# Kernel tuning notes

Measured on AMD Instinct MI355X. Metric: run time of the kernel, lower is better.

The kernel has to match this reference:

```python
import jax, jax.numpy as jnp
import numpy as np

N = 50000
E = 800000
HIDDEN = 128
NUM_HEADS = 8
D_HEAD = HIDDEN // NUM_HEADS


def setup_inputs() -> dict:
    key = jax.random.key(0)
    ks = jax.random.split(key, 12)
    sc = 1.0 / np.sqrt(HIDDEN)
    inp = {
        "h": jax.random.normal(ks[0], (N, HIDDEN), dtype=jnp.float32),
        "rows": jax.random.randint(ks[1], (E,), 0, N, dtype=jnp.int32),
        "cols": jax.random.randint(ks[2], (E,), 0, N, dtype=jnp.int32),
        "Wq": jax.random.normal(ks[3], (HIDDEN, HIDDEN), dtype=jnp.float32) * sc,
        "bq": jax.random.normal(ks[4], (HIDDEN,), dtype=jnp.float32) * sc,
        "Wk": jax.random.normal(ks[5], (HIDDEN, HIDDEN), dtype=jnp.float32) * sc,
        "bk": jax.random.normal(ks[6], (HIDDEN,), dtype=jnp.float32) * sc,
        "Wv": jax.random.normal(ks[7], (HIDDEN, HIDDEN), dtype=jnp.float32) * sc,
        "bv": jax.random.normal(ks[8], (HIDDEN,), dtype=jnp.float32) * sc,
        "Wo": jax.random.normal(ks[9], (HIDDEN, HIDDEN), dtype=jnp.float32) * sc,
        "bo": jax.random.normal(ks[10], (HIDDEN,), dtype=jnp.float32) * sc,
    }
    return inp


def reference(h, rows, cols, Wq, bq, Wk, bk, Wv, bv, Wo, bo):
    n = h.shape[0]
    scaling = D_HEAD ** (-0.5)
    # projections; torch-style reshape splits hidden as (d_head, num_heads)
    q = ((h @ Wq.T + bq).reshape(n, D_HEAD, NUM_HEADS)) * scaling
    k = (h @ Wk.T + bk).reshape(n, D_HEAD, NUM_HEADS)
    v = (h @ Wv.T + bv).reshape(n, D_HEAD, NUM_HEADS)
    # SDDMM: per-edge, per-head score = q[row] . k[col]   -> [E, H]
    scores = jnp.einsum("edh,edh->eh", q[rows], k[cols])
    # row-wise (destination) stable softmax over variable-degree neighborhoods
    m = jax.ops.segment_max(scores, rows, num_segments=n)  # [N, H]
    e = jnp.exp(scores - m[rows])
    s = jax.ops.segment_sum(e, rows, num_segments=n)  # [N, H]
    attn = e / s[rows]  # [E, H]
    # SpMM: out[i] = sum_{(i,j) in E} attn[e] * v[j]
    out = jax.ops.segment_sum(attn[:, None, :] * v[cols], rows, num_segments=n)
    return out.reshape(n, HIDDEN) @ Wo.T + bo
```

## Files before the change

### kernel.cpp

```cpp
#include <hip/hip_runtime.h>
#include <math.h>

#define N_NODES 50000
#define N_EDGES 800000
#define HID 128
#define CAP 64
#define EPT 8
#define SCAT_THREADS (N_EDGES / EPT)
#define SCAT_BLOCKS ((SCAT_THREADS + 255) / 256)
#define QKV_BLOCKS  ((N_NODES + 31) / 32)
#define ATTN_BLOCKS ((N_NODES + 3) / 4)
#define OUT_BLOCKS  ((N_NODES + 63) / 64)

typedef _Float16 f16_t;
typedef f16_t f16x8 __attribute__((ext_vector_type(8)));
typedef f16_t f16x2 __attribute__((ext_vector_type(2)));
typedef float f32x4 __attribute__((ext_vector_type(4)));

__device__ __forceinline__ ushort f2h_bits(float x) {
    union { f16_t h; ushort u; } c; c.h = (f16_t)x; return c.u;
}
__device__ __forceinline__ f16x2 as_h2(uint u) {
    union { uint u_; f16x2 h; } c; c.u_ = u; return c.h;
}
__device__ __forceinline__ f16x8 cvt8(const float* p) {
    float4 f0 = *(const float4*)p;
    float4 f1 = *(const float4*)(p + 4);
    f16x8 r;
    r[0] = (f16_t)f0.x; r[1] = (f16_t)f0.y; r[2] = (f16_t)f0.z; r[3] = (f16_t)f0.w;
    r[4] = (f16_t)f1.x; r[5] = (f16_t)f1.y; r[6] = (f16_t)f1.z; r[7] = (f16_t)f1.w;
    return r;
}

__global__ __launch_bounds__(256) void scatter(
    const int* __restrict__ rows, const int* __restrict__ cols,
    int* __restrict__ cnt, ushort* __restrict__ slots)
{
    const int t = blockIdx.x * 256 + threadIdx.x;
    if (t >= SCAT_THREADS) return;
    const int4* r4 = (const int4*)rows + (size_t)t * 2;
    const int4* c4 = (const int4*)cols + (size_t)t * 2;
    int4 ra = r4[0], rb = r4[1];
    int4 ca = c4[0], cb = c4[1];
    const int r[8] = {ra.x, ra.y, ra.z, ra.w, rb.x, rb.y, rb.z, rb.w};
    const int c[8] = {ca.x, ca.y, ca.z, ca.w, cb.x, cb.y, cb.z, cb.w};
    int p[8];
#pragma unroll
    for (int u = 0; u < 8; ++u)
        p[u] = atomicAdd(&cnt[r[u] << 4], 1);
#pragma unroll
    for (int u = 0; u < 8; ++u)
        if (p[u] < CAP) slots[(size_t)r[u] * CAP + p[u]] = (ushort)c[u];
}

__global__ __launch_bounds__(256) void gemm_qkv(
    const float* __restrict__ h,
    const float* __restrict__ Wq, const float* __restrict__ Wk,
    const float* __restrict__ Wv,
    const float* __restrict__ bq, const float* __restrict__ bk,
    const float* __restrict__ bv,
    uint* __restrict__ qp, uint2* __restrict__ kv)
{
    const int lane = threadIdx.x & 63;
    const int wid  = threadIdx.x >> 6;
    const int mrow = lane & 15;
    const int quad = lane >> 4;
    const int rb   = blockIdx.x * 32;

    f16x8 a[2][4];
#pragma unroll
    for (int s = 0; s < 2; ++s) {
        if (rb + s * 16 >= N_NODES) break;
        const float* src = h + (size_t)(rb + s * 16 + mrow) * HID + quad * 8;
#pragma unroll
        for (int kc = 0; kc < 4; ++kc) a[s][kc] = cvt8(src + kc * 32);
    }

    const int c0 = wid * 32 + mrow;
    const int c1 = c0 + 16;

    f16x8 bfr[2][4];
    f32x4 accq[2][2], acck[2][2], accv[2][2];

#define LOAD_B(W)                                                       \
    _Pragma("unroll")                                                   \
    for (int kc = 0; kc < 4; ++kc) {                                    \
        bfr[0][kc] = cvt8((W) + c0 * HID + kc * 32 + quad * 8);         \
        bfr[1][kc] = cvt8((W) + c1 * HID + kc * 32 + quad * 8);         \
    }
#define RUN_MFMA(dst)                                                   \
    _Pragma("unroll")                                                   \
    for (int s = 0; s < 2; ++s) {                                       \
        dst[s][0] = (f32x4){0.f, 0.f, 0.f, 0.f};                        \
        dst[s][1] = (f32x4){0.f, 0.f, 0.f, 0.f};                        \
        if (rb + s * 16 >= N_NODES) continue;                           \
        _Pragma("unroll")                                               \
        for (int kc = 0; kc < 4; ++kc) {                                \
            dst[s][0] = __builtin_amdgcn_mfma_f32_16x16x32_f16(         \
                a[s][kc], bfr[0][kc], dst[s][0], 0, 0, 0);              \
            dst[s][1] = __builtin_amdgcn_mfma_f32_16x16x32_f16(         \
                a[s][kc], bfr[1][kc], dst[s][1], 0, 0, 0);              \
        }                                                               \
    }

    LOAD_B(Wq); RUN_MFMA(accq);
    LOAD_B(Wk); RUN_MFMA(acck);
    LOAD_B(Wv); RUN_MFMA(accv);
#undef LOAD_B
#undef RUN_MFMA

    const float bq0 = bq[c0], bq1 = bq[c1];
    const float bk0 = bk[c0], bk1 = bk[c1];
    const float bv0 = bv[c0], bv1 = bv[c1];
    const bool  lo  = (mrow & 8) == 0;
    const int   i   = mrow & 7;

#pragma unroll
    for (int s = 0; s < 2; ++s) {
        if (rb + s * 16 >= N_NODES) break;
#pragma unroll
        for (int r = 0; r < 4; ++r) {
            const size_t orow = rb + s * 16 + quad * 4 + r;
            uint q0 = f2h_bits((accq[s][0][r] + bq0) * 0.25f);
            uint q1 = f2h_bits((accq[s][1][r] + bq1) * 0.25f);
            uint k0 = f2h_bits(acck[s][0][r] + bk0);
            uint k1 = f2h_bits(acck[s][1][r] + bk1);
            uint v0 = f2h_bits(accv[s][0][r] + bv0);
            uint v1 = f2h_bits(accv[s][1][r] + bv1);
            uint q0p = __shfl_xor(q0, 8), q1p = __shfl_xor(q1, 8);
            uint k0p = __shfl_xor(k0, 8), k1p = __shfl_xor(k1, 8);
            uint v0p = __shfl_xor(v0, 8), v1p = __shfl_xor(v1, 8);
            if (lo) {
                const size_t base = orow * 64 + 16 * wid + i;
                qp[base]     = q0 | (q0p << 16);
                qp[base + 8] = q1 | (q1p << 16);
                kv[base]     = make_uint2(k0 | (k0p << 16), v0 | (v0p << 16));
                kv[base + 8] = make_uint2(k1 | (k1p << 16), v1 | (v1p << 16));
            }
        }
    }
}

__device__ __forceinline__ void edge_acc(uint2 rr, f16x2 qh,
                                         float& l, float& Oa, float& Ob)
{
    float p = __builtin_amdgcn_fdot2(as_h2(rr.x), qh, 0.f, false);
    p += __shfl_xor(p, 8);
    p += __shfl_xor(p, 16);
    p += __shfl_xor(p, 32);
    float ex = __expf(p);
    f16x2 vh = as_h2(rr.y);
    l  += ex;
    Oa += ex * (float)vh[0];
    Ob += ex * (float)vh[1];
}

__global__ __launch_bounds__(256) void attn(
    const uint* __restrict__ qp, const uint2* __restrict__ kv,
    const int* __restrict__ cnt, const ushort* __restrict__ slots,
    ushort* __restrict__ ao)
{
    const int lane = threadIdx.x & 63;
    const int node = blockIdx.x * 4 + (threadIdx.x >> 6);
    if (node >= N_NODES) return;

    const f16x2 qh = as_h2(qp[(size_t)node * 64 + lane]);

    int deg = cnt[node << 4];
    if (deg > CAP) deg = CAP;
    const int myslot = (lane < deg) ? (int)slots[(size_t)node * CAP + lane] : 0;

    float ls[4] = {0.f, 0.f, 0.f, 0.f};
    float Oa[4] = {0.f, 0.f, 0.f, 0.f};
    float Ob[4] = {0.f, 0.f, 0.f, 0.f};

    int j = 0;
    for (; j + 4 <= deg; j += 4) {
        int s0 = __shfl(myslot, j);
        int s1 = __shfl(myslot, j + 1);
        int s2 = __shfl(myslot, j + 2);
        int s3 = __shfl(myslot, j + 3);
        uint2 r0 = kv[(size_t)s0 * 64 + lane];
        uint2 r1 = kv[(size_t)s1 * 64 + lane];
        uint2 r2 = kv[(size_t)s2 * 64 + lane];
        uint2 r3 = kv[(size_t)s3 * 64 + lane];
        edge_acc(r0, qh, ls[0], Oa[0], Ob[0]);
        edge_acc(r1, qh, ls[1], Oa[1], Ob[1]);
        edge_acc(r2, qh, ls[2], Oa[2], Ob[2]);
        edge_acc(r3, qh, ls[3], Oa[3], Ob[3]);
    }
    for (; j < deg; ++j) {
        int s = __shfl(myslot, j);
        uint2 rr = kv[(size_t)s * 64 + lane];
        edge_acc(rr, qh, ls[0], Oa[0], Ob[0]);
    }

    const float l  = (ls[0] + ls[1]) + (ls[2] + ls[3]);
    const float O0 = (Oa[0] + Oa[1]) + (Oa[2] + Oa[3]);
    const float O1 = (Ob[0] + Ob[1]) + (Ob[2] + Ob[3]);
    const float inv = (l > 0.f) ? 1.f / l : 0.f;

    const int ce = 32 * (lane >> 4) + 16 * ((lane >> 3) & 1) + (lane & 7);
    ao[(size_t)node * HID + ce]     = f2h_bits(O0 * inv);
    ao[(size_t)node * HID + ce + 8] = f2h_bits(O1 * inv);
}

__global__ __launch_bounds__(256) void gemm_out(
    const ushort* __restrict__ A, const float* __restrict__ Wo,
    const float* __restrict__ bias, float* __restrict__ out)
{
    const int lane = threadIdx.x & 63;
    const int wid  = threadIdx.x >> 6;
    const int mrow = lane & 15;
    const int quad = lane >> 4;
    const int rb   = blockIdx.x * 64;

    const int c0 = wid * 32 + mrow;
    const int c1 = c0 + 16;

    f16x8 bfr[2][4];
#pragma unroll
    for (int kc = 0; kc < 4; ++kc) {
        bfr[0][kc] = cvt8(Wo + c0 * HID + kc * 32 + quad * 8);
        bfr[1][kc] = cvt8(Wo + c1 * HID + kc * 32 + quad * 8);
    }

    f32x4 acc[4][2];
#pragma unroll
    for (int s = 0; s < 4; ++s) {
        acc[s][0] = (f32x4){0.f, 0.f, 0.f, 0.f};
        acc[s][1] = (f32x4){0.f, 0.f, 0.f, 0.f};
    }

#pragma unroll
    for (int s = 0; s < 4; ++s) {
        if (rb + s * 16 >= N_NODES) break;
        const ushort* ap = A + (size_t)(rb + s * 16 + mrow) * HID + quad * 8;
        f16x8 a0 = *(const f16x8*)(ap);
        f16x8 a1 = *(const f16x8*)(ap + 32);
        f16x8 a2 = *(const f16x8*)(ap + 64);
        f16x8 a3 = *(const f16x8*)(ap + 96);
        acc[s][0] = __builtin_amdgcn_mfma_f32_16x16x32_f16(a0, bfr[0][0], acc[s][0], 0, 0, 0);
        acc[s][1] = __builtin_amdgcn_mfma_f32_16x16x32_f16(a0, bfr[1][0], acc[s][1], 0, 0, 0);
        acc[s][0] = __builtin_amdgcn_mfma_f32_16x16x32_f16(a1, bfr[0][1], acc[s][0], 0, 0, 0);
        acc[s][1] = __builtin_amdgcn_mfma_f32_16x16x32_f16(a1, bfr[1][1], acc[s][1], 0, 0, 0);
        acc[s][0] = __builtin_amdgcn_mfma_f32_16x16x32_f16(a2, bfr[0][2], acc[s][0], 0, 0, 0);
        acc[s][1] = __builtin_amdgcn_mfma_f32_16x16x32_f16(a2, bfr[1][2], acc[s][1], 0, 0, 0);
        acc[s][0] = __builtin_amdgcn_mfma_f32_16x16x32_f16(a3, bfr[0][3], acc[s][0], 0, 0, 0);
        acc[s][1] = __builtin_amdgcn_mfma_f32_16x16x32_f16(a3, bfr[1][3], acc[s][1], 0, 0, 0);
    }

#pragma unroll
    for (int t = 0; t < 2; ++t) {
        const int c = (t == 0) ? c0 : c1;
        const float bc = bias[c];
#pragma unroll
        for (int s = 0; s < 4; ++s) {
            if (rb + s * 16 >= N_NODES) break;
#pragma unroll
            for (int r = 0; r < 4; ++r) {
                const size_t orow = rb + s * 16 + quad * 4 + r;
                out[orow * HID + c] = acc[s][t][r] + bc;
            }
        }
    }
}

extern "C" void kernel_launch(void* const* d_in, const int* in_sizes, int n_in,
                              void* d_out, int out_size, void* d_ws, size_t ws_size,
                              hipStream_t stream)
{
    const float* h    = (const float*)d_in[0];
    const int*   rows = (const int*)  d_in[1];
    const int*   cols = (const int*)  d_in[2];
    const float* Wq   = (const float*)d_in[3];
    const float* bq   = (const float*)d_in[4];
    const float* Wk   = (const float*)d_in[5];
    const float* bk   = (const float*)d_in[6];
    const float* Wv   = (const float*)d_in[7];
    const float* bv   = (const float*)d_in[8];
    const float* Wo   = (const float*)d_in[9];
    const float* bo   = (const float*)d_in[10];
    float* out = (float*)d_out;

    char* ws = (char*)d_ws;
    uint*   qp    = (uint*)ws;    ws += (size_t)N_NODES * 64 * 4;
    uint2*  kv    = (uint2*)ws;   ws += (size_t)N_NODES * 64 * 8;
    ushort* ao    = (ushort*)ws;  ws += (size_t)N_NODES * HID * 2;
    int*    cnt   = (int*)ws;     ws += (size_t)N_NODES * 64;
    ushort* slots = (ushort*)ws;

    hipMemsetAsync(cnt, 0, (size_t)N_NODES * 64, stream);

    dim3 blk(256);
    scatter<<<SCAT_BLOCKS, blk, 0, stream>>>(rows, cols, cnt, slots);
    gemm_qkv<<<QKV_BLOCKS, blk, 0, stream>>>(h, Wq, Wk, Wv, bq, bk, bv, qp, kv);
    attn<<<ATTN_BLOCKS, blk, 0, stream>>>(qp, kv, cnt, slots, ao);
    gemm_out<<<OUT_BLOCKS, blk, 0, stream>>>(ao, Wo, bo, out);
}
```

Measured before the change: 256.1 us.

## Fuse fp16 pre-conversion of h and weights into scatter prep kernel, split QKV GEMM

Adds a combined prep kernel that runs the edge scatter alongside fp16 conversion of h and all four weight matrices, so the GEMMs load fp16 directly instead of converting fp32 on the fly. The QKV GEMM gets a second grid dimension so each wave computes one 16-column tile across Q, K and V, which doubles the block count and changes the per-wave output layout. The attention output column mapping is adjusted to match. The cost is an extra fp16 copy of h written to and read back from the workspace, and the QKV kernel now reloads the A tile once per y-block.

```diff
diff --git a/kernel.cpp b/kernel.cpp
--- a/kernel.cpp
+++ b/kernel.cpp
@@ -5,12 +5,16 @@
 #define N_EDGES 800000
 #define HID 128
 #define CAP 64
-#define EPT 8
-#define SCAT_THREADS (N_EDGES / EPT)
-#define SCAT_BLOCKS ((SCAT_THREADS + 255) / 256)
-#define QKV_BLOCKS  ((N_NODES + 31) / 32)
-#define ATTN_BLOCKS ((N_NODES + 3) / 4)
-#define OUT_BLOCKS  ((N_NODES + 63) / 64)
+
+#define SCAT_TH   (N_EDGES / 8)
+#define SCAT_BLK  ((SCAT_TH + 255) / 256)
+#define WCVT_BLK  64
+#define HCVT_BLK  (N_NODES * HID / 4 / 256)
+#define PREP_BLK  (SCAT_BLK + WCVT_BLK + HCVT_BLK)
+
+#define QKV_BX    ((N_NODES + 31) / 32)
+#define ATTN_BLK  ((N_NODES + 3) / 4)
+#define OUT_BLK   ((N_NODES + 63) / 64)
 
 typedef _Float16 f16_t;
 typedef f16_t f16x8 __attribute__((ext_vector_type(8)));
@@ -23,40 +27,56 @@
 __device__ __forceinline__ f16x2 as_h2(uint u) {
     union { uint u_; f16x2 h; } c; c.u_ = u; return c.h;
 }
-__device__ __forceinline__ f16x8 cvt8(const float* p) {
-    float4 f0 = *(const float4*)p;
-    float4 f1 = *(const float4*)(p + 4);
-    f16x8 r;
-    r[0] = (f16_t)f0.x; r[1] = (f16_t)f0.y; r[2] = (f16_t)f0.z; r[3] = (f16_t)f0.w;
-    r[4] = (f16_t)f1.x; r[5] = (f16_t)f1.y; r[6] = (f16_t)f1.z; r[7] = (f16_t)f1.w;
-    return r;
-}
-
-__global__ __launch_bounds__(256) void scatter(
+
+__global__ __launch_bounds__(256) void prep(
+    const float* __restrict__ h,
+    const float* __restrict__ Wq, const float* __restrict__ Wk,
+    const float* __restrict__ Wv, const float* __restrict__ Wo,
+    ushort* __restrict__ hf, ushort* __restrict__ wf,
     const int* __restrict__ rows, const int* __restrict__ cols,
     int* __restrict__ cnt, ushort* __restrict__ slots)
 {
-    const int t = blockIdx.x * 256 + threadIdx.x;
-    if (t >= SCAT_THREADS) return;
-    const int4* r4 = (const int4*)rows + (size_t)t * 2;
-    const int4* c4 = (const int4*)cols + (size_t)t * 2;
-    int4 ra = r4[0], rb = r4[1];
-    int4 ca = c4[0], cb = c4[1];
-    const int r[8] = {ra.x, ra.y, ra.z, ra.w, rb.x, rb.y, rb.z, rb.w};
-    const int c[8] = {ca.x, ca.y, ca.z, ca.w, cb.x, cb.y, cb.z, cb.w};
-    int p[8];
-#pragma unroll
-    for (int u = 0; u < 8; ++u)
-        p[u] = atomicAdd(&cnt[r[u] << 4], 1);
-#pragma unroll
-    for (int u = 0; u < 8; ++u)
-        if (p[u] < CAP) slots[(size_t)r[u] * CAP + p[u]] = (ushort)c[u];
+    const int b = blockIdx.x;
+    const int tid = threadIdx.x;
+
+    if (b < SCAT_BLK) {
+        const int t = b * 256 + tid;
+        if (t < SCAT_TH) {
+            const int4* r4 = (const int4*)rows + (size_t)t * 2;
+            const int4* c4 = (const int4*)cols + (size_t)t * 2;
+            int4 ra = r4[0], rb2 = r4[1];
+            int4 ca = c4[0], cb = c4[1];
+            const int r[8] = {ra.x, ra.y, ra.z, ra.w, rb2.x, rb2.y, rb2.z, rb2.w};
+            const int c[8] = {ca.x, ca.y, ca.z, ca.w, cb.x, cb.y, cb.z, cb.w};
+            int p[8];
+#pragma unroll
+            for (int u = 0; u < 8; ++u)
+                p[u] = atomicAdd(&cnt[r[u] << 4], 1);
+#pragma unroll
+            for (int u = 0; u < 8; ++u)
+                if (p[u] < CAP) slots[(size_t)r[u] * CAP + p[u]] = (ushort)c[u];
+        }
+    } else if (b < SCAT_BLK + WCVT_BLK) {
+        const int t = (b - SCAT_BLK) * 256 + tid;
+        const int m = t >> 12, i = t & 4095;
+        const float* src = (m == 0) ? Wq : (m == 1) ? Wk : (m == 2) ? Wv : Wo;
+        float4 f = ((const float4*)src)[i];
+        ushort4 o;
+        o.x = f2h_bits(f.x); o.y = f2h_bits(f.y);
+        o.z = f2h_bits(f.z); o.w = f2h_bits(f.w);
+        ((ushort4*)(wf + m * 16384))[i] = o;
+    } else {
+        const int t = (b - SCAT_BLK - WCVT_BLK) * 256 + tid;
+        float4 f = ((const float4*)h)[t];
+        ushort4 o;
+        o.x = f2h_bits(f.x); o.y = f2h_bits(f.y);
+        o.z = f2h_bits(f.z); o.w = f2h_bits(f.w);
+        ((ushort4*)hf)[t] = o;
+    }
 }
 
 __global__ __launch_bounds__(256) void gemm_qkv(
-    const float* __restrict__ h,
-    const float* __restrict__ Wq, const float* __restrict__ Wk,
-    const float* __restrict__ Wv,
+    const ushort* __restrict__ hf, const ushort* __restrict__ wf,
     const float* __restrict__ bq, const float* __restrict__ bk,
     const float* __restrict__ bv,
     uint* __restrict__ qp, uint2* __restrict__ kv)
@@ -66,79 +86,63 @@
     const int mrow = lane & 15;
     const int quad = lane >> 4;
     const int rb   = blockIdx.x * 32;
+    const int T    = blockIdx.y * 4 + wid;
+    const int c    = T * 16 + mrow;
 
     f16x8 a[2][4];
 #pragma unroll
     for (int s = 0; s < 2; ++s) {
-        if (rb + s * 16 >= N_NODES) break;
-        const float* src = h + (size_t)(rb + s * 16 + mrow) * HID + quad * 8;
-#pragma unroll
-        for (int kc = 0; kc < 4; ++kc) a[s][kc] = cvt8(src + kc * 32);
-    }
-
-    const int c0 = wid * 32 + mrow;
-    const int c1 = c0 + 16;
-
-    f16x8 bfr[2][4];
-    f32x4 accq[2][2], acck[2][2], accv[2][2];
-
-#define LOAD_B(W)                                                       \
-    _Pragma("unroll")                                                   \
-    for (int kc = 0; kc < 4; ++kc) {                                    \
-        bfr[0][kc] = cvt8((W) + c0 * HID + kc * 32 + quad * 8);         \
-        bfr[1][kc] = cvt8((W) + c1 * HID + kc * 32 + quad * 8);         \
-    }
-#define RUN_MFMA(dst)                                                   \
-    _Pragma("unroll")                                                   \
-    for (int s = 0; s < 2; ++s) {                                       \
-        dst[s][0] = (f32x4){0.f, 0.f, 0.f, 0.f};                        \
-        dst[s][1] = (f32x4){0.f, 0.f, 0.f, 0.f};                        \
-        if (rb + s * 16 >= N_NODES) continue;                           \
-        _Pragma("unroll")                                               \
-        for (int kc = 0; kc < 4; ++kc) {                                \
-            dst[s][0] = __builtin_amdgcn_mfma_f32_16x16x32_f16(         \
-                a[s][kc], bfr[0][kc], dst[s][0], 0, 0, 0);              \
-            dst[s][1] = __builtin_amdgcn_mfma_f32_16x16x32_f16(         \
-                a[s][kc], bfr[1][kc], dst[s][1], 0, 0, 0);              \
-        }                                                               \
-    }
-
-    LOAD_B(Wq); RUN_MFMA(accq);
-    LOAD_B(Wk); RUN_MFMA(acck);
-    LOAD_B(Wv); RUN_MFMA(accv);
-#undef LOAD_B
-#undef RUN_MFMA
-
-    const float bq0 = bq[c0], bq1 = bq[c1];
-    const float bk0 = bk[c0], bk1 = bk[c1];
-    const float bv0 = bv[c0], bv1 = bv[c1];
+        int ar = rb + s * 16 + mrow;
+        if (ar >= N_NODES) ar = N_NODES - 1;
+        const ushort* ap = hf + (size_t)ar * HID + quad * 8;
+#pragma unroll
+        for (int kc = 0; kc < 4; ++kc) a[s][kc] = *(const f16x8*)(ap + kc * 32);
+    }
+    f16x8 bQ[4], bK[4], bV[4];
+#pragma unroll
+    for (int kc = 0; kc < 4; ++kc) {
+        const int off = c * HID + kc * 32 + quad * 8;
+        bQ[kc] = *(const f16x8*)(wf + off);
+        bK[kc] = *(const f16x8*)(wf + 16384 + off);
+        bV[kc] = *(const f16x8*)(wf + 32768 + off);
+    }
+
+    f32x4 aq[2], ak[2], av[2];
+#pragma unroll
+    for (int s = 0; s < 2; ++s) {
+        aq[s] = (f32x4){0.f, 0.f, 0.f, 0.f};
+        ak[s] = (f32x4){0.f, 0.f, 0.f, 0.f};
+        av[s] = (f32x4){0.f, 0.f, 0.f, 0.f};
+    }
+#pragma unroll
+    for (int s = 0; s < 2; ++s)
+#pragma unroll
+        for (int kc = 0; kc < 4; ++kc) {
+            aq[s] = __builtin_amdgcn_mfma_f32_16x16x32_f16(a[s][kc], bQ[kc], aq[s], 0, 0, 0);
+            ak[s] = __builtin_amdgcn_mfma_f32_16x16x32_f16(a[s][kc], bK[kc], ak[s], 0, 0, 0);
+            av[s] = __builtin_amdgcn_mfma_f32_16x16x32_f16(a[s][kc], bV[kc], av[s], 0, 0, 0);
+        }
+
+    const float bqc = bq[c], bkc = bk[c], bvc = bv[c];
     const bool  lo  = (mrow & 8) == 0;
     const int   i   = mrow & 7;
-
-#pragma unroll
-    for (int s = 0; s < 2; ++s) {
-        if (rb + s * 16 >= N_NODES) break;
+#pragma unroll
+    for (int s = 0; s < 2; ++s)
 #pragma unroll
         for (int r = 0; r < 4; ++r) {
-            const size_t orow = rb + s * 16 + quad * 4 + r;
-            uint q0 = f2h_bits((accq[s][0][r] + bq0) * 0.25f);
-            uint q1 = f2h_bits((accq[s][1][r] + bq1) * 0.25f);
-            uint k0 = f2h_bits(acck[s][0][r] + bk0);
-            uint k1 = f2h_bits(acck[s][1][r] + bk1);
-            uint v0 = f2h_bits(accv[s][0][r] + bv0);
-            uint v1 = f2h_bits(accv[s][1][r] + bv1);
-            uint q0p = __shfl_xor(q0, 8), q1p = __shfl_xor(q1, 8);
-            uint k0p = __shfl_xor(k0, 8), k1p = __shfl_xor(k1, 8);
-            uint v0p = __shfl_xor(v0, 8), v1p = __shfl_xor(v1, 8);
-            if (lo) {
-                const size_t base = orow * 64 + 16 * wid + i;
-                qp[base]     = q0 | (q0p << 16);
-                qp[base + 8] = q1 | (q1p << 16);
-                kv[base]     = make_uint2(k0 | (k0p << 16), v0 | (v0p << 16));
-                kv[base + 8] = make_uint2(k1 | (k1p << 16), v1 | (v1p << 16));
+            const int orow = rb + s * 16 + quad * 4 + r;
+            uint qv = f2h_bits((aq[s][r] + bqc) * 0.25f);
+            uint kb = f2h_bits(ak[s][r] + bkc);
+            uint vb = f2h_bits(av[s][r] + bvc);
+            uint qh = __shfl_xor((int)qv, 8);
+            uint kh = __shfl_xor((int)kb, 8);
+            uint vh = __shfl_xor((int)vb, 8);
+            if (lo && orow < N_NODES) {
+                const size_t base = (size_t)orow * 64 + 8 * T + i;
+                qp[base] = qv | (qh << 16);
+                kv[base] = make_uint2(kb | (kh << 16), vb | (vh << 16));
             }
         }
-    }
 }
 
 __device__ __forceinline__ void edge_acc(uint2 rr, f16x2 qh,
@@ -200,13 +204,13 @@
     const float O1 = (Ob[0] + Ob[1]) + (Ob[2] + Ob[3]);
     const float inv = (l > 0.f) ? 1.f / l : 0.f;
 
-    const int ce = 32 * (lane >> 4) + 16 * ((lane >> 3) & 1) + (lane & 7);
+    const int ce = 16 * (lane >> 3) + (lane & 7);
     ao[(size_t)node * HID + ce]     = f2h_bits(O0 * inv);
     ao[(size_t)node * HID + ce + 8] = f2h_bits(O1 * inv);
 }
 
 __global__ __launch_bounds__(256) void gemm_out(
-    const ushort* __restrict__ A, const float* __restrict__ Wo,
+    const ushort* __restrict__ A, const ushort* __restrict__ wfo,
     const float* __restrict__ bias, float* __restrict__ out)
 {
     const int lane = threadIdx.x & 63;
@@ -218,11 +222,20 @@
     const int c0 = wid * 32 + mrow;
     const int c1 = c0 + 16;
 
-    f16x8 bfr[2][4];
+    f16x8 a[4][4];
+#pragma unroll
+    for (int s = 0; s < 4; ++s) {
+        int ar = rb + s * 16 + mrow;
+        if (ar >= N_NODES) ar = N_NODES - 1;
+        const ushort* ap = A + (size_t)ar * HID + quad * 8;
+#pragma unroll
+        for (int kc = 0; kc < 4; ++kc) a[s][kc] = *(const f16x8*)(ap + kc * 32);
+    }
+    f16x8 b0[4], b1[4];
 #pragma unroll
     for (int kc = 0; kc < 4; ++kc) {
-        bfr[0][kc] = cvt8(Wo + c0 * HID + kc * 32 + quad * 8);
-        bfr[1][kc] = cvt8(Wo + c1 * HID + kc * 32 + quad * 8);
+        b0[kc] = *(const f16x8*)(wfo + c0 * HID + kc * 32 + quad * 8);
+        b1[kc] = *(const f16x8*)(wfo + c1 * HID + kc * 32 + quad * 8);
     }
 
     f32x4 acc[4][2];
@@ -231,39 +244,25 @@
         acc[s][0] = (f32x4){0.f, 0.f, 0.f, 0.f};
         acc[s][1] = (f32x4){0.f, 0.f, 0.f, 0.f};
     }
-
-#pragma unroll
-    for (int s = 0; s < 4; ++s) {
-        if (rb + s * 16 >= N_NODES) break;
-        const ushort* ap = A + (size_t)(rb + s * 16 + mrow) * HID + quad * 8;
-        f16x8 a0 = *(const f16x8*)(ap);
-        f16x8 a1 = *(const f16x8*)(ap + 32);
-        f16x8 a2 = *(const f16x8*)(ap + 64);
-        f16x8 a3 = *(const f16x8*)(ap + 96);
-        acc[s][0] = __builtin_amdgcn_mfma_f32_16x16x32_f16(a0, bfr[0][0], acc[s][0], 0, 0, 0);
-        acc[s][1] = __builtin_amdgcn_mfma_f32_16x16x32_f16(a0, bfr[1][0], acc[s][1], 0, 0, 0);
-        acc[s][0] = __builtin_amdgcn_mfma_f32_16x16x32_f16(a1, bfr[0][1], acc[s][0], 0, 0, 0);
-        acc[s][1] = __builtin_amdgcn_mfma_f32_16x16x32_f16(a1, bfr[1][1], acc[s][1], 0, 0, 0);
-        acc[s][0] = __builtin_amdgcn_mfma_f32_16x16x32_f16(a2, bfr[0][2], acc[s][0], 0, 0, 0);
-        acc[s][1] = __builtin_amdgcn_mfma_f32_16x16x32_f16(a2, bfr[1][2], acc[s][1], 0, 0, 0);
-        acc[s][0] = __builtin_amdgcn_mfma_f32_16x16x32_f16(a3, bfr[0][3], acc[s][0], 0, 0, 0);
-        acc[s][1] = __builtin_amdgcn_mfma_f32_16x16x32_f16(a3, bfr[1][3], acc[s][1], 0, 0, 0);
-    }
-
-#pragma unroll
-    for (int t = 0; t < 2; ++t) {
-        const int c = (t == 0) ? c0 : c1;
-        const float bc = bias[c];
-#pragma unroll
-        for (int s = 0; s < 4; ++s) {
-            if (rb + s * 16 >= N_NODES) break;
-#pragma unroll
-            for (int r = 0; r < 4; ++r) {
-                const size_t orow = rb + s * 16 + quad * 4 + r;
-                out[orow * HID + c] = acc[s][t][r] + bc;
+#pragma unroll
+    for (int s = 0; s < 4; ++s)
+#pragma unroll
+        for (int kc = 0; kc < 4; ++kc) {
+            acc[s][0] = __builtin_amdgcn_mfma_f32_16x16x32_f16(a[s][kc], b0[kc], acc[s][0], 0, 0, 0);
+            acc[s][1] = __builtin_amdgcn_mfma_f32_16x16x32_f16(a[s][kc], b1[kc], acc[s][1], 0, 0, 0);
+        }
+
+    const float bc0 = bias[c0], bc1 = bias[c1];
+#pragma unroll
+    for (int s = 0; s < 4; ++s)
+#pragma unroll
+        for (int r = 0; r < 4; ++r) {
+            const int orow = rb + s * 16 + quad * 4 + r;
+            if (orow < N_NODES) {
+                out[(size_t)orow * HID + c0] = acc[s][0][r] + bc0;
+                out[(size_t)orow * HID + c1] = acc[s][1][r] + bc1;
             }
         }
-    }
 }
 
 extern "C" void kernel_launch(void* const* d_in, const int* in_sizes, int n_in,
@@ -286,15 +285,18 @@
     char* ws = (char*)d_ws;
     uint*   qp    = (uint*)ws;    ws += (size_t)N_NODES * 64 * 4;
     uint2*  kv    = (uint2*)ws;   ws += (size_t)N_NODES * 64 * 8;
+    ushort* hf    = (ushort*)ws;  ws += (size_t)N_NODES * HID * 2;
     ushort* ao    = (ushort*)ws;  ws += (size_t)N_NODES * HID * 2;
+    ushort* wf    = (ushort*)ws;  ws += 4 * 16384 * 2;
     int*    cnt   = (int*)ws;     ws += (size_t)N_NODES * 64;
     ushort* slots = (ushort*)ws;
 
     hipMemsetAsync(cnt, 0, (size_t)N_NODES * 64, stream);
 
     dim3 blk(256);
-    scatter<<<SCAT_BLOCKS, blk, 0, stream>>>(rows, cols, cnt, slots);
-    gemm_qkv<<<QKV_BLOCKS, blk, 0, stream>>>(h, Wq, Wk, Wv, bq, bk, bv, qp, kv);
-    attn<<<ATTN_BLOCKS, blk, 0, stream>>>(qp, kv, cnt, slots, ao);
-    gemm_out<<<OUT_BLOCKS, blk, 0, stream>>>(ao, Wo, bo, out);
-}
+    prep<<<PREP_BLK, blk, 0, stream>>>(h, Wq, Wk, Wv, Wo, hf, wf,
+                                       rows, cols, cnt, slots);
+    gemm_qkv<<<dim3(QKV_BX, 2), blk, 0, stream>>>(hf, wf, bq, bk, bv, qp, kv);
+    attn<<<ATTN_BLK, blk, 0, stream>>>(qp, kv, cnt, slots, ao);
+    gemm_out<<<OUT_BLK, blk, 0, stream>>>(ao, wf + 3 * 16384, bo, out);
+}
```

Measured after the change: 234.6 us. 8.4% less time.
